# Kernel tuning notes

Measured on AMD Instinct MI355X. Metric: run time of the kernel, lower is better.

Reference implementation:

```python
import jax, jax.numpy as jnp
import numpy as np

N = 1024       # sentence length (words incl. root at index 0)
WD = 300       # word embedding dim (GloVe-style)
PD = 25        # pos_emb_dim
H = 125        # hidden_dim_lstm
FC = 100       # hidden_dim_fc
PVOCAB = 50    # POS tagset size


def setup_inputs() -> dict:
    key = jax.random.key(0)
    ks = jax.random.split(key, 14)
    f = lambda k, s: jax.random.normal(k, s, dtype=jnp.float32) * 0.1
    d_in = WD + PD
    return {
        "word_vecs": jax.random.normal(ks[0], (N, WD), dtype=jnp.float32),
        "pos_idx": jax.random.randint(ks[1], (N,), 0, PVOCAB),
        "parents_ids": jax.random.randint(ks[2], (N,), 0, N),
        "pos_emb": f(ks[3], (PVOCAB, PD)),
        "Wih0": f(ks[4], (2, 4 * H, d_in)),
        "Whh0": f(ks[5], (2, 4 * H, H)),
        "b0": f(ks[6], (2, 4 * H)),
        "Wih1": f(ks[7], (2, 4 * H, 2 * H)),
        "Whh1": f(ks[8], (2, 4 * H, H)),
        "b1": f(ks[9], (2, 4 * H)),
        "fc1_W": f(ks[10], (FC, 4 * H)),
        "fc1_b": f(ks[11], (FC,)),
        "fc2_W": f(ks[12], (1, FC)),
        "fc2_b": f(ks[13], (1,)),
    }


def _lstm_dir(x, Wih, Whh, b, reverse):
    # torch LSTM cell, gate order (i, f, g, o); b = b_ih + b_hh
    Hd = Whh.shape[1]
    def step(carry, xt):
        h, c = carry
        g = xt @ Wih.T + h @ Whh.T + b
        i, fg, gg, o = jnp.split(g, 4)
        i = jax.nn.sigmoid(i)
        fg = jax.nn.sigmoid(fg)
        gg = jnp.tanh(gg)
        o = jax.nn.sigmoid(o)
        c = fg * c + i * gg
        h = o * jnp.tanh(c)
        return (h, c), h
    init = (jnp.zeros((Hd,), x.dtype), jnp.zeros((Hd,), x.dtype))
    _, hs = jax.lax.scan(step, init, x, reverse=reverse)
    return hs  # [n, H], already in original time order


def _bilstm_layer(x, Wih, Whh, b):
    hf = _lstm_dir(x, Wih[0], Whh[0], b[0], False)
    hb = _lstm_dir(x, Wih[1], Whh[1], b[1], True)
    return jnp.concatenate([hf, hb], axis=1)  # [n, 2H]


def reference(word_vecs, pos_idx, parents_ids, pos_emb, Wih0, Whh0, b0,
              Wih1, Whh1, b1, fc1_W, fc1_b, fc2_W, fc2_b):
    # encoder: concat word + pos embeddings, 2-layer BiLSTM
    x = jnp.concatenate([word_vecs, pos_emb[pos_idx]], axis=1)  # [n, WD+PD]
    h = _bilstm_layer(x, Wih0, Whh0, b0)
    h = _bilstm_layer(h, Wih1, Whh1, b1)  # [n, 2H]
    n = h.shape[0]
    twoH = h.shape[1]
    # fc1(cat(h_i, h_j)) = h_i @ W_head^T + h_j @ W_child^T + b  (vectorized over all pairs)
    A = h @ fc1_W[:, :twoH].T   # head contribution  [n, FC]
    B = h @ fc1_W[:, twoH:].T   # child contribution [n, FC]
    T = jnp.tanh(A[:, None, :] + B[None, :, :] + fc1_b)  # [n, n, FC]
    raw = T @ fc2_W[0] + fc2_b[0]                         # [n, n]
    ii = jnp.arange(n)
    # original loop skips diagonal and arcs into the root (j == 0); those stay 0
    mask = (ii[:, None] != ii[None, :]) & (ii[None, :] != 0)
    scores_mat = jnp.where(mask, raw, jnp.float32(0.0))
    logits = scores_mat.T  # row j = scores of heads for child j
    logp = jax.nn.log_softmax(logits, axis=1)
    loss = -jnp.mean(logp[jnp.arange(n), parents_ids])
    return loss, scores_mat
```

## Files before the change

kernel.cpp:

```cpp
#include <hip/hip_runtime.h>

typedef float v2f __attribute__((ext_vector_type(2)));
typedef _Float16 f16x8 __attribute__((ext_vector_type(8)));
typedef float f32x4 __attribute__((ext_vector_type(4)));

#define LOG2E 1.4426950408889634f
#define LN2   0.6931471805599453f

__device__ __forceinline__ float fexp2(float x) {
  float r; asm("v_exp_f32 %0, %1" : "=v"(r) : "v"(x)); return r;
}
__device__ __forceinline__ float frcp(float x) {
  float r; asm("v_rcp_f32 %0, %1" : "=v"(r) : "v"(x)); return r;
}
__device__ __forceinline__ float flog2(float x) {
  float r; asm("v_log_f32 %0, %1" : "=v"(r) : "v"(x)); return r;
}
__device__ __forceinline__ void lgkm_barrier() {
  __builtin_amdgcn_sched_barrier(0);
  asm volatile("s_waitcnt lgkmcnt(0)" ::: "memory");
  __builtin_amdgcn_s_barrier();
  __builtin_amdgcn_sched_barrier(0);
}

__global__ void k_embed(const float* __restrict__ wv, const int* __restrict__ pidx,
                        const float* __restrict__ pemb, float* __restrict__ X) {
  int t = blockIdx.x;
  int pi = pidx[t];
  for (int c = threadIdx.x; c < 336; c += 128) {
    float v;
    if (c < 300)      v = wv[t * 300 + c];
    else if (c < 325) v = pemb[pi * 25 + (c - 300)];
    else              v = 0.f;
    X[t * 336 + c] = v;
  }
}

__global__ void k_wpack(const float* __restrict__ Wih, const float* __restrict__ b,
                        float* __restrict__ Wp, float* __restrict__ bp,
                        int sK, int dK) {
  const int d = blockIdx.y, rho = blockIdx.x;
  const int u = rho >> 2, g = rho & 3;
  const bool ok = (u < 125);
  const float* src = Wih + ((size_t)d * 500 + g * 125 + (ok ? u : 0)) * sK;
  float* dst = Wp + ((size_t)d * 512 + rho) * dK;
  for (int c = threadIdx.x; c < dK; c += 128)
    dst[c] = (ok && c < sK) ? src[c] : 0.f;
  if (threadIdx.x == 0)
    bp[d * 512 + rho] = ok ? b[d * 500 + g * 125 + u] : 0.f;
}

__global__ void k_wab(const float* __restrict__ fc1W, float* __restrict__ Wab) {
  int r = blockIdx.x;
  int sr = (r < 100) ? r : r - 100;
  int so = (r < 100) ? 0 : 250;
  for (int c = threadIdx.x; c < 256; c += 128)
    Wab[r * 256 + c] = (c < 250) ? fc1W[sr * 500 + so + c] : 0.f;
}

__global__ void k_misc(const float* __restrict__ fc1b, const float* __restrict__ fc2W,
                       float* __restrict__ biasAB, float* __restrict__ sumw) {
  __shared__ float red[128];
  int t = threadIdx.x;
  for (int c = t; c < 256; c += 128)
    biasAB[c] = (c < 100) ? fc1b[c] : 0.f;
  float s = (t < 100) ? fc2W[t] : 0.f;
  red[t] = s; __syncthreads();
  for (int off = 64; off; off >>= 1) {
    if (t < off) red[t] += red[t + off];
    __syncthreads();
  }
  if (t == 0) sumw[0] = red[0];
}

#define BM 64
#define BN 64
#define BKK 16
__global__ __launch_bounds__(256) void k_gemm(
    const float* __restrict__ A, const float* __restrict__ Bw,
    const float* __restrict__ bias, float* __restrict__ C,
    int M, int N, int K, int ldC, long sBz, long sCz, long sbz, int transOut) {
  const int z = blockIdx.z;
  const float* Bp = Bw + (size_t)z * sBz;
  const float* bp = bias + (size_t)z * sbz;
  float* Cp = C + (size_t)z * sCz;
  const int bm = blockIdx.y * BM, bn = blockIdx.x * BN;
  __shared__ __align__(16) float As[BKK][BM + 4];
  __shared__ __align__(16) float Bs[BKK][BN + 4];
  __shared__ float Ts[BN][BM + 1];
  const int tid = threadIdx.x;
  const int tx = tid & 15, ty = tid >> 4;
  const int lr = tid >> 2;
  const int lk = (tid & 3) * 4;
  float acc[4][4];
#pragma unroll
  for (int a = 0; a < 4; ++a)
#pragma unroll
    for (int b = 0; b < 4; ++b) acc[a][b] = 0.f;

  int brow = bn + lr; if (brow >= N) brow = N - 1;
  for (int k0 = 0; k0 < K; k0 += BKK) {
    float4 a4 = *(const float4*)(A + (size_t)(bm + lr) * K + k0 + lk);
    float4 b4 = *(const float4*)(Bp + (size_t)brow * K + k0 + lk);
    __syncthreads();
    As[lk + 0][lr] = a4.x; As[lk + 1][lr] = a4.y; As[lk + 2][lr] = a4.z; As[lk + 3][lr] = a4.w;
    Bs[lk + 0][lr] = b4.x; Bs[lk + 1][lr] = b4.y; Bs[lk + 2][lr] = b4.z; Bs[lk + 3][lr] = b4.w;
    __syncthreads();
#pragma unroll
    for (int kk = 0; kk < BKK; ++kk) {
      float4 av = *(const float4*)&As[kk][ty * 4];
      float4 bv = *(const float4*)&Bs[kk][tx * 4];
      float aa[4] = {av.x, av.y, av.z, av.w};
      float bb[4] = {bv.x, bv.y, bv.z, bv.w};
#pragma unroll
      for (int a = 0; a < 4; ++a)
#pragma unroll
        for (int b = 0; b < 4; ++b)
          acc[a][b] = __builtin_fmaf(aa[a], bb[b], acc[a][b]);
    }
  }
  if (!transOut) {
#pragma unroll
    for (int a = 0; a < 4; ++a) {
      int i = bm + ty * 4 + a;
#pragma unroll
      for (int b = 0; b < 4; ++b) {
        int j = bn + tx * 4 + b;
        if (j < N) Cp[(size_t)i * ldC + j] = acc[a][b] + bp[j];
      }
    }
  } else {
    __syncthreads();
#pragma unroll
    for (int a = 0; a < 4; ++a)
#pragma unroll
      for (int b = 0; b < 4; ++b) {
        int jn = bn + tx * 4 + b; if (jn >= N) jn = N - 1;
        Ts[tx * 4 + b][ty * 4 + a] = acc[a][b] + bp[jn];
      }
    __syncthreads();
    const int n2 = tid >> 2, mq = (tid & 3) * 16;
    const int n = bn + n2;
    if (n < N) {
#pragma unroll
      for (int r = 0; r < 4; ++r) {
        int m0 = mq + r * 4;
        float4 v;
        v.x = Ts[n2][m0 + 0]; v.y = Ts[n2][m0 + 1];
        v.z = Ts[n2][m0 + 2]; v.w = Ts[n2][m0 + 3];
        *(float4*)(Cp + (size_t)n * ldC + bm + m0) = v;
      }
    }
  }
}

__global__ __launch_bounds__(1024) void k_rec(const float* __restrict__ Ptt,
                                              const float* __restrict__ Whh,
                                              float* __restrict__ hout) {
  const int d = blockIdx.x;
  const bool fwd = (d == 0);
  const int t = threadIdx.x;
  const int w  = t >> 6;
  const int l  = t & 63;
  const int lg = l >> 4;
  const int lc = l & 15;
  const int rtsel = lc & 1;

  const float* Wd = Whh + (size_t)d * 500 * 125;
  f16x8 a[2][4];
#pragma unroll
  for (int rt = 0; rt < 2; ++rt) {
    const int rho = (w << 5) + (rt << 4) + lc;
    const int u2 = rho >> 2, g2 = rho & 3;
    const bool uok = (u2 < 125);
    const float* wr2 = Wd + (size_t)(g2 * 125 + (uok ? u2 : 0)) * 125;
#pragma unroll
    for (int kt = 0; kt < 4; ++kt) {
      f16x8 v;
#pragma unroll
      for (int j = 0; j < 8; ++j) {
        const int k = kt * 32 + lg * 8 + j;
        v[j] = (_Float16)((uok && k < 125) ? wr2[k] : 0.f);
      }
      a[rt][kt] = v;
    }
  }

  __shared__ __align__(16) _Float16 hf[2][128];
  __shared__ float hist[32][128];
  if (t < 128) ((int*)hf)[t] = 0;

  const int dstep = fwd ? 512 : -512;
  const float* pg = Ptt + (size_t)d * 1024 * 512 +
                    (size_t)(fwd ? 0 : 1023) * 512 + ((w << 5) + (lg << 2));
  f32x4 pc0 = *(const f32x4*)(pg);
  f32x4 pc1 = *(const f32x4*)(pg + 16);
  pg += dstep;
  float cst = 0.f;
  __syncthreads();

  for (int cb = 0; cb < 128; ++cb) {
#pragma unroll
    for (int e = 0; e < 8; ++e) {
      const int buf = e & 1;
      f32x4 pn0 = *(const f32x4*)(pg);
      f32x4 pn1 = *(const f32x4*)(pg + 16);
      pg += dstep;
      f16x8 hfr[4];
#pragma unroll
      for (int kt = 0; kt < 4; ++kt)
        hfr[kt] = *(const f16x8*)&hf[buf][kt * 32 + lg * 8];
      f32x4 acc0 = pc0, acc1 = pc1;
#pragma unroll
      for (int kt = 0; kt < 4; ++kt) {
        acc0 = __builtin_amdgcn_mfma_f32_16x16x32_f16(a[0][kt], hfr[kt], acc0, 0, 0, 0);
        acc1 = __builtin_amdgcn_mfma_f32_16x16x32_f16(a[1][kt], hfr[kt], acc1, 0, 0, 0);
      }
      f32x4 T = rtsel ? acc1 : acc0;
      float gi = frcp(1.f + fexp2(-LOG2E * T[0]));
      float gf = frcp(1.f + fexp2(-LOG2E * T[1]));
      float gg = __builtin_fmaf(2.f, frcp(1.f + fexp2(-2.f * LOG2E * T[2])), -1.f);
      float go = frcp(1.f + fexp2(-LOG2E * T[3]));
      cst = __builtin_fmaf(gf, cst, gi * gg);
      float th = __builtin_fmaf(2.f, frcp(1.f + fexp2(-2.f * LOG2E * cst)), -1.f);
      float hv = go * th;
      const int u_own = (w << 3) + (rtsel << 2) + lg;
      if (lc < 2 && u_own < 125) {
        hf[buf ^ 1][u_own] = (_Float16)hv;
        hist[(cb & 3) * 8 + e][u_own] = hv;
      }
      lgkm_barrier();
      pc0 = pn0; pc1 = pn1;
    }
    if ((cb & 3) == 3) {
      const int S0 = (cb - 3) * 8;
#pragma unroll
      for (int k = 0; k < 4; ++k) {
        int idx = t + k * 1024;
        int r = idx >> 7, u2 = idx & 127;
        if (u2 < 125) {
          int step = S0 + r;
          int time = fwd ? step : 1023 - step;
          hout[(size_t)time * 256 + d * 125 + u2] = hist[r][u2];
        }
      }
      lgkm_barrier();
    }
  }
}

__global__ __launch_bounds__(256) void k_pair(const float* __restrict__ AB,
    const float* __restrict__ fc2W, const float* __restrict__ fc2b,
    const float* __restrict__ sumw, float* __restrict__ outS,
    float* __restrict__ scoresT) {
  __shared__ float As[32][100];
  __shared__ float Bs[32][101];
  __shared__ float w2s[100];
  const int tid = threadIdx.x;
  const int i0 = blockIdx.y * 32, j0 = blockIdx.x * 32;
  for (int idx = tid; idx < 3200; idx += 256) {
    int r = idx / 100, k = idx - r * 100;
    As[r][k] = AB[(size_t)(i0 + r) * 200 + k];
    Bs[r][k] = AB[(size_t)(j0 + r) * 200 + 100 + k];
  }
  if (tid < 100) w2s[tid] = 2.f * fc2W[tid];
  __syncthreads();
  const int tx = tid & 31, ty = tid >> 5;
  float acc[4] = {0.f, 0.f, 0.f, 0.f};
#pragma unroll 4
  for (int k = 0; k < 100; ++k) {
    float b = Bs[tx][k];
    float wk2 = w2s[k];
    float bs = b * (2.f * LOG2E);
#pragma unroll
    for (int q = 0; q < 4; ++q) {
      float a = As[ty + 8 * q][k];
      float r = frcp(1.f + fexp2(__builtin_fmaf(a, 2.f * LOG2E, bs)));
      acc[q] = __builtin_fmaf(wk2, r, acc[q]);
    }
  }
  float base = sumw[0] + fc2b[0];
  const int j = j0 + tx;
#pragma unroll
  for (int q = 0; q < 4; ++q) {
    int i = i0 + ty + 8 * q;
    float val = (i != j && j != 0) ? (base - acc[q]) : 0.f;
    outS[(size_t)i * 1024 + j] = val;
    scoresT[(size_t)j * 1024 + i] = val;
  }
}

__global__ __launch_bounds__(256) void k_soft(const float* __restrict__ scoresT,
    const int* __restrict__ parents, float* __restrict__ contrib) {
  const int j = blockIdx.x, tid = threadIdx.x;
  __shared__ float red[256];
  const float* row = scoresT + (size_t)j * 1024;
  float v0 = row[tid], v1 = row[tid + 256], v2 = row[tid + 512], v3 = row[tid + 768];
  float m = fmaxf(fmaxf(v0, v1), fmaxf(v2, v3));
  red[tid] = m; __syncthreads();
  for (int off = 128; off; off >>= 1) {
    if (tid < off) red[tid] = fmaxf(red[tid], red[tid + off]);
    __syncthreads();
  }
  m = red[0]; __syncthreads();
  float s = fexp2((v0 - m) * LOG2E) + fexp2((v1 - m) * LOG2E) +
            fexp2((v2 - m) * LOG2E) + fexp2((v3 - m) * LOG2E);
  red[tid] = s; __syncthreads();
  for (int off = 128; off; off >>= 1) {
    if (tid < off) red[tid] += red[tid + off];
    __syncthreads();
  }
  if (tid == 0) {
    float S = red[0];
    int p = parents[j];
    contrib[j] = row[p] - m - flog2(S) * LN2;
  }
}

__global__ __launch_bounds__(256) void k_loss(const float* __restrict__ contrib,
                                              float* __restrict__ out) {
  __shared__ float red[256];
  int tid = threadIdx.x;
  float s = contrib[tid] + contrib[tid + 256] + contrib[tid + 512] + contrib[tid + 768];
  red[tid] = s; __syncthreads();
  for (int off = 128; off; off >>= 1) {
    if (tid < off) red[tid] += red[tid + off];
    __syncthreads();
  }
  if (tid == 0) out[0] = -red[0] * (1.f / 1024.f);
}

extern "C" void kernel_launch(void* const* d_in, const int* in_sizes, int n_in,
                              void* d_out, int out_size, void* d_ws, size_t ws_size,
                              hipStream_t stream) {
  const float* wv   = (const float*)d_in[0];
  const int*   pidx = (const int*)d_in[1];
  const int*   par  = (const int*)d_in[2];
  const float* pemb = (const float*)d_in[3];
  const float* Wih0 = (const float*)d_in[4];
  const float* Whh0 = (const float*)d_in[5];
  const float* b0   = (const float*)d_in[6];
  const float* Wih1 = (const float*)d_in[7];
  const float* Whh1 = (const float*)d_in[8];
  const float* b1   = (const float*)d_in[9];
  const float* fc1W = (const float*)d_in[10];
  const float* fc1b = (const float*)d_in[11];
  const float* fc2W = (const float*)d_in[12];
  const float* fc2b = (const float*)d_in[13];
  float* ws = (float*)d_ws;
  float* X      = ws + 0;
  float* Wih0p  = ws + 344064;
  float* Wih1p  = ws + 688128;
  float* brho0  = ws + 950272;
  float* brho1  = ws + 951296;
  float* Ptt    = ws + 952320;
  float* h0     = ws + 2000896;
  float* h1     = ws + 2263040;
  float* Wab    = ws + 2525184;
  float* biasAB = ws + 2576384;
  float* AB     = ws + 2576640;
  float* scT    = ws + 2781440;
  float* contrib= ws + 3830016;
  float* sumw   = ws + 3831040;
  float* out = (float*)d_out;

  hipMemsetAsync(h0, 0, 1024 * 256 * sizeof(float), stream);
  hipMemsetAsync(h1, 0, 1024 * 256 * sizeof(float), stream);

  k_embed <<<1024, 128, 0, stream>>>(wv, pidx, pemb, X);
  k_wpack <<<dim3(512, 2), 128, 0, stream>>>(Wih0, b0, Wih0p, brho0, 325, 336);
  k_wpack <<<dim3(512, 2), 128, 0, stream>>>(Wih1, b1, Wih1p, brho1, 250, 256);
  k_wab   <<<200, 128, 0, stream>>>(fc1W, Wab);
  k_misc  <<<1, 128, 0, stream>>>(fc1b, fc2W, biasAB, sumw);

  k_gemm<<<dim3(8, 16, 2), 256, 0, stream>>>(X, Wih0p, brho0, Ptt, 1024, 512, 336, 512,
                                             512L * 336, 1024L * 512, 512L, 0);
  k_rec <<<2, 1024, 0, stream>>>(Ptt, Whh0, h0);
  k_gemm<<<dim3(8, 16, 2), 256, 0, stream>>>(h0, Wih1p, brho1, Ptt, 1024, 512, 256, 512,
                                             512L * 256, 1024L * 512, 512L, 0);
  k_rec <<<2, 1024, 0, stream>>>(Ptt, Whh1, h1);
  k_gemm<<<dim3(4, 16, 1), 256, 0, stream>>>(h1, Wab, biasAB, AB, 1024, 200, 256, 200,
                                             0L, 0L, 0L, 0);
  k_pair<<<dim3(32, 32), 256, 0, stream>>>(AB, fc2W, fc2b, sumw, out + 1, scT);
  k_soft<<<1024, 256, 0, stream>>>(scT, par, contrib);
  k_loss<<<1, 256, 0, stream>>>(contrib, out);
}
```

Before: 1.269 ms.

## Halve recurrent LSTM block to 8 waves with 4 MFMA row tiles each

The recurrent kernel now runs 512 threads (8 waves) instead of 1024, and each wave computes four 16-row gate tiles instead of two, so fewer waves take part in the per-step barrier. The history buffer and its periodic batch flush to global memory are removed. Each step's hidden value is now written straight to global memory, and the next step's precomputed input projection is loaded into the accumulators directly. The goal is a shorter serial per-timestep critical path through cheaper barriers and less LDS traffic. The cost is twice the MFMA work per wave per step, plus scattered small global stores on every step.

```diff
diff --git a/kernel.cpp b/kernel.cpp
--- a/kernel.cpp
+++ b/kernel.cpp
@@ -154,9 +154,9 @@
   }
 }
 
-__global__ __launch_bounds__(1024) void k_rec(const float* __restrict__ Ptt,
-                                              const float* __restrict__ Whh,
-                                              float* __restrict__ hout) {
+__global__ __launch_bounds__(512) void k_rec(const float* __restrict__ Ptt,
+                                             const float* __restrict__ Whh,
+                                             float* __restrict__ hout) {
   const int d = blockIdx.x;
   const bool fwd = (d == 0);
   const int t = threadIdx.x;
@@ -164,13 +164,13 @@
   const int l  = t & 63;
   const int lg = l >> 4;
   const int lc = l & 15;
-  const int rtsel = lc & 1;
+  const int q  = lc >> 2;
 
   const float* Wd = Whh + (size_t)d * 500 * 125;
-  f16x8 a[2][4];
-#pragma unroll
-  for (int rt = 0; rt < 2; ++rt) {
-    const int rho = (w << 5) + (rt << 4) + lc;
+  f16x8 a[4][4];
+#pragma unroll
+  for (int rt = 0; rt < 4; ++rt) {
+    const int rho = (w << 6) + (rt << 4) + lc;
     const int u2 = rho >> 2, g2 = rho & 3;
     const bool uok = (u2 < 125);
     const float* wr2 = Wd + (size_t)(g2 * 125 + (uok ? u2 : 0)) * 125;
@@ -187,65 +187,56 @@
   }
 
   __shared__ __align__(16) _Float16 hf[2][128];
-  __shared__ float hist[32][128];
   if (t < 128) ((int*)hf)[t] = 0;
 
   const int dstep = fwd ? 512 : -512;
   const float* pg = Ptt + (size_t)d * 1024 * 512 +
-                    (size_t)(fwd ? 0 : 1023) * 512 + ((w << 5) + (lg << 2));
-  f32x4 pc0 = *(const f32x4*)(pg);
-  f32x4 pc1 = *(const f32x4*)(pg + 16);
+                    (size_t)(fwd ? 0 : 1023) * 512 + ((w << 6) + (lg << 2));
+  f32x4 acc[4];
+#pragma unroll
+  for (int rt = 0; rt < 4; ++rt)
+    acc[rt] = *(const f32x4*)(pg + rt * 16);
   pg += dstep;
+
+  const int u_own = (w << 4) + (q << 2) + lg;
+  const bool wr = ((lc & 3) == 0) && (u_own < 125);
+  float* ho = hout + (size_t)(fwd ? 0 : 1023) * 256 + d * 125 + u_own;
+  const int hstep = fwd ? 256 : -256;
+
   float cst = 0.f;
   __syncthreads();
 
-  for (int cb = 0; cb < 128; ++cb) {
-#pragma unroll
-    for (int e = 0; e < 8; ++e) {
-      const int buf = e & 1;
-      f32x4 pn0 = *(const f32x4*)(pg);
-      f32x4 pn1 = *(const f32x4*)(pg + 16);
-      pg += dstep;
-      f16x8 hfr[4];
-#pragma unroll
-      for (int kt = 0; kt < 4; ++kt)
-        hfr[kt] = *(const f16x8*)&hf[buf][kt * 32 + lg * 8];
-      f32x4 acc0 = pc0, acc1 = pc1;
-#pragma unroll
-      for (int kt = 0; kt < 4; ++kt) {
-        acc0 = __builtin_amdgcn_mfma_f32_16x16x32_f16(a[0][kt], hfr[kt], acc0, 0, 0, 0);
-        acc1 = __builtin_amdgcn_mfma_f32_16x16x32_f16(a[1][kt], hfr[kt], acc1, 0, 0, 0);
-      }
-      f32x4 T = rtsel ? acc1 : acc0;
-      float gi = frcp(1.f + fexp2(-LOG2E * T[0]));
-      float gf = frcp(1.f + fexp2(-LOG2E * T[1]));
-      float gg = __builtin_fmaf(2.f, frcp(1.f + fexp2(-2.f * LOG2E * T[2])), -1.f);
-      float go = frcp(1.f + fexp2(-LOG2E * T[3]));
-      cst = __builtin_fmaf(gf, cst, gi * gg);
-      float th = __builtin_fmaf(2.f, frcp(1.f + fexp2(-2.f * LOG2E * cst)), -1.f);
-      float hv = go * th;
-      const int u_own = (w << 3) + (rtsel << 2) + lg;
-      if (lc < 2 && u_own < 125) {
-        hf[buf ^ 1][u_own] = (_Float16)hv;
-        hist[(cb & 3) * 8 + e][u_own] = hv;
-      }
-      lgkm_barrier();
-      pc0 = pn0; pc1 = pn1;
-    }
-    if ((cb & 3) == 3) {
-      const int S0 = (cb - 3) * 8;
-#pragma unroll
-      for (int k = 0; k < 4; ++k) {
-        int idx = t + k * 1024;
-        int r = idx >> 7, u2 = idx & 127;
-        if (u2 < 125) {
-          int step = S0 + r;
-          int time = fwd ? step : 1023 - step;
-          hout[(size_t)time * 256 + d * 125 + u2] = hist[r][u2];
-        }
-      }
-      lgkm_barrier();
-    }
+#pragma unroll 2
+  for (int s = 0; s < 1024; ++s) {
+    const int buf = s & 1;
+    f16x8 hfr[4];
+#pragma unroll
+    for (int kt = 0; kt < 4; ++kt)
+      hfr[kt] = *(const f16x8*)&hf[buf][kt * 32 + lg * 8];
+#pragma unroll
+    for (int kt = 0; kt < 4; ++kt)
+#pragma unroll
+      for (int rt = 0; rt < 4; ++rt)
+        acc[rt] = __builtin_amdgcn_mfma_f32_16x16x32_f16(a[rt][kt], hfr[kt],
+                                                         acc[rt], 0, 0, 0);
+    f32x4 T = (q == 0) ? acc[0] : (q == 1) ? acc[1] : (q == 2) ? acc[2] : acc[3];
+#pragma unroll
+    for (int rt = 0; rt < 4; ++rt)
+      acc[rt] = *(const f32x4*)(pg + rt * 16);
+    pg += dstep;
+    float gi = frcp(1.f + fexp2(-LOG2E * T[0]));
+    float gf = frcp(1.f + fexp2(-LOG2E * T[1]));
+    float gg = __builtin_fmaf(2.f, frcp(1.f + fexp2(-2.f * LOG2E * T[2])), -1.f);
+    float go = frcp(1.f + fexp2(-LOG2E * T[3]));
+    cst = __builtin_fmaf(gf, cst, gi * gg);
+    float th = __builtin_fmaf(2.f, frcp(1.f + fexp2(-2.f * LOG2E * cst)), -1.f);
+    float hv = go * th;
+    if (wr) {
+      hf[buf ^ 1][u_own] = (_Float16)hv;
+      *ho = hv;
+    }
+    ho += hstep;
+    lgkm_barrier();
   }
 }
 
@@ -375,10 +366,10 @@
 
   k_gemm<<<dim3(8, 16, 2), 256, 0, stream>>>(X, Wih0p, brho0, Ptt, 1024, 512, 336, 512,
                                              512L * 336, 1024L * 512, 512L, 0);
-  k_rec <<<2, 1024, 0, stream>>>(Ptt, Whh0, h0);
+  k_rec <<<2, 512, 0, stream>>>(Ptt, Whh0, h0);
   k_gemm<<<dim3(8, 16, 2), 256, 0, stream>>>(h0, Wih1p, brho1, Ptt, 1024, 512, 256, 512,
                                              512L * 256, 1024L * 512, 512L, 0);
-  k_rec <<<2, 1024, 0, stream>>>(Ptt, Whh1, h1);
+  k_rec <<<2, 512, 0, stream>>>(Ptt, Whh1, h1);
   k_gemm<<<dim3(4, 16, 1), 256, 0, stream>>>(h1, Wab, biasAB, AB, 1024, 200, 256, 200,
                                              0L, 0L, 0L, 0);
   k_pair<<<dim3(32, 32), 256, 0, stream>>>(AB, fc2W, fc2b, sumw, out + 1, scT);
```

Result: slower. 1.322 ms (+4.2%).
